# Kernel optimization log

Hardware: AMD Instinct MI355X
Metric: run time of the kernel (lower is better)

## Reference

```python
import jax, jax.numpy as jnp
import numpy as np

NE = 64        # num experts
H = 1024       # hidden_size
F = 2048       # ffn_hidden_size per expert
T = 16384      # total tokens


def setup_inputs() -> dict:
    key = jax.random.key(0)
    k1, k2, k3 = jax.random.split(key, 3)
    x = jax.random.normal(k1, (T, H), jnp.float32)
    w1 = jax.random.normal(k2, (NE, F, H), jnp.float32) * 0.02
    w2 = jax.random.normal(k3, (NE, F, H), jnp.float32) * 0.02
    # ragged token counts per expert, summing exactly to T
    rng = np.random.default_rng(0)
    sizes = rng.multinomial(T, np.ones(NE) / NE)
    tokens_per_expert = jnp.asarray(sizes, jnp.int32)
    return {"x": x, "w1": w1, "w2": w2, "tokens_per_expert": tokens_per_expert}


def _grouped_gmm(x, w, sizes, trans_b=False):
    # grouped GEMM: per-expert segment of x multiplied by that expert's weight.
    # sizes are concrete host ints (group boundaries are static), so we emit
    # one GEMM per expert with static slices, matching gg.ops.gmm semantics.
    offs = np.concatenate([[0], np.cumsum(sizes)]).astype(np.int64)
    outs = []
    for e in range(len(sizes)):
        xe = x[int(offs[e]):int(offs[e + 1])]          # [n_e, k]
        we = w[e].T if trans_b else w[e]               # [k, n]
        outs.append(xe @ we)
    return jnp.concatenate(outs, axis=0)


def reference(x, w1, w2, tokens_per_expert):
    sizes = np.asarray(tokens_per_expert)
    h = _grouped_gmm(x, w1, sizes, trans_b=True)       # [T, F]
    h = jax.nn.gelu(h, approximate=False)              # torch F.gelu (exact erf)
    return _grouped_gmm(h, w2, sizes, trans_b=False)   # [T, H]
```

## Files before the change

### kernel.cpp

```cpp
#include <hip/hip_runtime.h>
#include <hip/hip_bf16.h>

#define NE 64
#define HDIM 1024
#define FDIM 2048
#define TDIM 16384

typedef __attribute__((ext_vector_type(8))) short short8;
typedef __attribute__((ext_vector_type(4))) float f32x4;
typedef unsigned short u16;
typedef unsigned int u32;

struct IC0 { static constexpr int v = 0; };
struct IC1 { static constexpr int v = 1; };
template<int W> struct WN { static constexpr int v = W; };

__device__ __forceinline__ u16 f2bf(float f) {
  return __bfloat16_as_ushort(__float2bfloat16(f));
}
__device__ __forceinline__ u32 pk2(float a, float b) {
  return (u32)f2bf(a) | ((u32)f2bf(b) << 16);
}
template<int N> __device__ __forceinline__ void waitv() {
  if constexpr (N == 2)       asm volatile("s_waitcnt vmcnt(2)" ::: "memory");
  else if constexpr (N == 8)  asm volatile("s_waitcnt vmcnt(8)" ::: "memory");
  else if constexpr (N == 10) asm volatile("s_waitcnt vmcnt(10)" ::: "memory");
}
__device__ __forceinline__ void waitl() {
  asm volatile("s_waitcnt lgkmcnt(0)" ::: "memory");
}

__global__ void k_prep(const int* __restrict__ tpe, int4* __restrict__ map,
                       int* __restrict__ nblocks) {
  if (threadIdx.x != 0 || blockIdx.x != 0) return;
  int off = 0, nb = 0;
  for (int e = 0; e < NE; ++e) {
    int n = tpe[e];
    for (int r = 0; r < n; r += 256) {
      int re = (r + 256 < n) ? (r + 256) : n;
      map[nb++] = make_int4(e, off + r, off + re, 0);
    }
    off += n;
  }
  *nblocks = nb;
}

__global__ void k_conv(const float4* __restrict__ in, uint2* __restrict__ out, int n4) {
  int stride = gridDim.x * blockDim.x;
  for (int i = blockIdx.x * blockDim.x + threadIdx.x; i < n4; i += stride) {
    float4 v = in[i];
    uint2 o;
    o.x = pk2(v.x, v.y);
    o.y = pk2(v.z, v.w);
    out[i] = o;
  }
}

template<int K, int N, int NY>
__global__ __launch_bounds__(512) void k_gemm1(
    const u16* __restrict__ A, const float* __restrict__ Bf, u16* __restrict__ C,
    const int4* __restrict__ map, const int* __restrict__ nblocks)
{
  const int mblk = (int)blockIdx.x / NY;
  const int nblk = (int)blockIdx.x % NY;
  if (mblk >= *nblocks) return;
  const int4 mi = map[mblk];
  const int e = mi.x, row0 = mi.y, rowend = mi.z;
  const int n0 = nblk << 7;
  const int NT = K / 32;

  __shared__ __align__(16) u16   sa[2][8192];
  __shared__ __align__(16) float sbf[3][4096];

  const int tid = threadIdx.x;
  const int wid = tid >> 6, lane = tid & 63;
  const int wr = wid >> 1, wc = wid & 1;
  const int fr = lane & 15, fq = lane >> 4;

  f32x4 acc[4][4];
#pragma unroll
  for (int m = 0; m < 4; ++m)
#pragma unroll
    for (int n = 0; n < 4; ++n) acc[m][n] = (f32x4)0.f;

  const float* B = Bf + (size_t)e * ((size_t)N * K);

  auto issueA = [&](int t, int buf) {
#pragma unroll
    for (int i = 0; i < 2; ++i) {
      int slot = i * 512 + tid;
      int r = slot >> 2, c = slot & 3;
      int cs = c ^ ((r >> 1) & 3);
      int row = row0 + r;
      row = row < TDIM ? row : TDIM - 1;
      const u16* g = A + (size_t)row * K + t * 32 + cs * 8;
      __builtin_amdgcn_global_load_lds(
          (const __attribute__((address_space(1))) u32*)g,
          (__attribute__((address_space(3))) u32*)(&sa[buf][i * 4096 + wid * 512]),
          16, 0, 0);
    }
  };
  auto issueB = [&](int t, int buf) {
#pragma unroll
    for (int i = 0; i < 2; ++i) {
      int slot = i * 512 + tid;
      int nn = slot >> 3, p = slot & 7;
      int cs = p ^ (nn & 7);
      const float* g = B + (size_t)(n0 + nn) * K + t * 32 + cs * 4;
      __builtin_amdgcn_global_load_lds(
          (const __attribute__((address_space(1))) u32*)g,
          (__attribute__((address_space(3))) u32*)(&sbf[buf][i * 2048 + wid * 256]),
          16, 0, 0);
    }
  };

  auto body = [&](int t) {
    waitv<2>();
    __builtin_amdgcn_s_barrier();
    const int curA = t & 1, curB = t % 3;
    issueA((t + 1 < NT) ? (t + 1) : (NT - 1), curA ^ 1);
    issueB((t + 2 < NT) ? (t + 2) : (NT - 1), (t + 2) % 3);
    short8 av[4], bv[4];
#pragma unroll
    for (int m = 0; m < 4; ++m) {
      const int row = wr * 64 + m * 16 + fr;
      av[m] = *(const short8*)(&sa[curA][row * 32 + (fq ^ ((row >> 1) & 3)) * 8]);
    }
#pragma unroll
    for (int n = 0; n < 4; ++n) {
      const int nn = wc * 64 + n * 16 + fr;
      const int swz = nn & 7;
      float4 lo = *(const float4*)(&sbf[curB][nn * 32 + ((fq * 2 + 0) ^ swz) * 4]);
      float4 hi = *(const float4*)(&sbf[curB][nn * 32 + ((fq * 2 + 1) ^ swz) * 4]);
      union { short8 s; u32 u[4]; } bb;
      bb.u[0] = pk2(lo.x, lo.y); bb.u[1] = pk2(lo.z, lo.w);
      bb.u[2] = pk2(hi.x, hi.y); bb.u[3] = pk2(hi.z, hi.w);
      bv[n] = bb.s;
    }
#pragma unroll
    for (int m = 0; m < 4; ++m)
#pragma unroll
      for (int n = 0; n < 4; ++n)
        acc[m][n] = __builtin_amdgcn_mfma_f32_16x16x32_bf16(av[m], bv[n], acc[m][n], 0, 0, 0);
  };

  issueA(0, 0);
  issueB(0, 0);
  issueB(1, 1);
  for (int t = 0; t < NT; ++t) body(t);

#pragma unroll
  for (int m = 0; m < 4; ++m) {
    const int rb = row0 + wr * 64 + m * 16 + fq * 4;
#pragma unroll
    for (int n = 0; n < 4; ++n) {
      const int col = n0 + wc * 64 + n * 16 + fr;
#pragma unroll
      for (int j = 0; j < 4; ++j) {
        int r = rb + j;
        if (r < rowend) {
          float vv = acc[m][n][j];
          vv = 0.5f * vv * (1.f + erff(vv * 0.70710678118654752f));
          C[(size_t)r * N + col] = f2bf(vv);
        }
      }
    }
  }
}

template<int K, int N, int NY>
__global__ __launch_bounds__(512) void k_gemm2(
    const u16* __restrict__ A, const float* __restrict__ Bf, float* __restrict__ C,
    const int4* __restrict__ map, const int* __restrict__ nblocks)
{
  const int mblk = (int)blockIdx.x / NY;
  const int nblk = (int)blockIdx.x % NY;
  if (mblk >= *nblocks) return;
  const int4 mi = map[mblk];
  const int e = mi.x, row0 = mi.y, rowend = mi.z;
  const int n0 = nblk << 7;
  const int NT = K / 32;
  constexpr int LB = 8;

  __shared__ __align__(16) u16 sa[3][8192];
  __shared__ __align__(16) u16 sb[2][128 * 40];

  const int tid = threadIdx.x;
  const int wid = tid >> 6, lane = tid & 63;
  const int wr = wid >> 1, wc = wid & 1;
  const int fr = lane & 15, fq = lane >> 4;

  f32x4 acc[4][4];
#pragma unroll
  for (int m = 0; m < 4; ++m)
#pragma unroll
    for (int n = 0; n < 4; ++n) acc[m][n] = (f32x4)0.f;

  const float* B = Bf + (size_t)e * ((size_t)N * K);

  float rb2[2][8];
  const int bn  = tid & 127;
  const int oct = tid >> 7;

  auto issueA = [&](int t, int buf) {
#pragma unroll
    for (int i = 0; i < 2; ++i) {
      int slot = i * 512 + tid;
      int r = slot >> 2, c = slot & 3;
      int cs = c ^ ((r >> 1) & 3);
      int row = row0 + r;
      row = row < TDIM ? row : TDIM - 1;
      const u16* g = A + (size_t)row * K + t * 32 + cs * 8;
      __builtin_amdgcn_global_load_lds(
          (const __attribute__((address_space(1))) u32*)g,
          (__attribute__((address_space(3))) u32*)(&sa[buf][i * 4096 + wid * 512]),
          16, 0, 0);
    }
  };
  auto loadB = [&](int t, auto ic) {
    constexpr int S = decltype(ic)::v;
    const float* src = B + (size_t)(t * 32 + oct * 8) * N + n0 + bn;
#pragma unroll
    for (int i = 0; i < 8; ++i) rb2[S][i] = src[(size_t)i * N];
  };
  auto writeB = [&](int buf, auto ic) {
    constexpr int S = decltype(ic)::v;
    uint4 c;
    c.x = pk2(rb2[S][0], rb2[S][1]); c.y = pk2(rb2[S][2], rb2[S][3]);
    c.z = pk2(rb2[S][4], rb2[S][5]); c.w = pk2(rb2[S][6], rb2[S][7]);
    *(uint4*)(&sb[buf][bn * 40 + oct * 8]) = c;
  };

  auto body = [&](int t, auto icCur, auto wn) {
    waitv<decltype(wn)::v>();
    waitl();
    __builtin_amdgcn_s_barrier();
    const int cur3 = t % 3, curb = t & 1, nxtb = curb ^ 1;
    short8 av[4], bv[4];
#pragma unroll
    for (int m = 0; m < 4; ++m) {
      const int row = wr * 64 + m * 16 + fr;
      av[m] = *(const short8*)(&sa[cur3][row * 32 + (fq ^ ((row >> 1) & 3)) * 8]);
    }
#pragma unroll
    for (int n = 0; n < 4; ++n)
      bv[n] = *(const short8*)(&sb[curb][(wc * 64 + n * 16 + fr) * 40 + fq * 8]);
    issueA((t + 2 < NT) ? (t + 2) : (NT - 1), (t + 2) % 3);
    writeB(nxtb, icCur);
    loadB((t + 3 < NT) ? (t + 3) : (NT - 1), icCur);
#pragma unroll
    for (int m = 0; m < 4; ++m)
#pragma unroll
      for (int n = 0; n < 4; ++n)
        acc[m][n] = __builtin_amdgcn_mfma_f32_16x16x32_bf16(av[m], bv[n], acc[m][n], 0, 0, 0);
  };

  issueA(0, 0);
  loadB(0, IC0{});
  issueA(1, 1);
  loadB(1, IC1{});
  waitv<2 + LB>();
  writeB(0, IC0{});
  loadB(2, IC0{});

  body(0, IC1{}, WN<LB>{});
  body(1, IC0{}, WN<2 + LB>{});
  for (int t = 2; t < NT; t += 2) {
    body(t,     IC1{}, WN<2 + LB>{});
    body(t + 1, IC0{}, WN<2 + LB>{});
  }

#pragma unroll
  for (int m = 0; m < 4; ++m) {
    const int rb = row0 + wr * 64 + m * 16 + fq * 4;
#pragma unroll
    for (int n = 0; n < 4; ++n) {
      const int col = n0 + wc * 64 + n * 16 + fr;
#pragma unroll
      for (int j = 0; j < 4; ++j) {
        int r = rb + j;
        if (r < rowend) C[(size_t)r * N + col] = acc[m][n][j];
      }
    }
  }
}

extern "C" void kernel_launch(void* const* d_in, const int* in_sizes, int n_in,
                              void* d_out, int out_size, void* d_ws, size_t ws_size,
                              hipStream_t stream) {
  const float* x  = (const float*)d_in[0];
  const float* w1 = (const float*)d_in[1];
  const float* w2 = (const float*)d_in[2];
  const int*  tpe = (const int*)d_in[3];

  char* ws = (char*)d_ws;
  int4* map     = (int4*)ws;
  int*  nblocks = (int*)(ws + 4096);
  u16*  xb      = (u16*)(ws + 8192);
  u16*  hb      = xb + (size_t)TDIM * HDIM;

  k_prep<<<1, 64, 0, stream>>>(tpe, map, nblocks);
  k_conv<<<2048, 256, 0, stream>>>((const float4*)x, (uint2*)xb, (TDIM * HDIM) / 4);
  k_gemm1<HDIM, FDIM, 16><<<128 * 16, 512, 0, stream>>>(
      xb, w1, hb, map, nblocks);
  k_gemm2<FDIM, HDIM, 8><<<128 * 8, 512, 0, stream>>>(
      hb, w2, (float*)d_out, map, nblocks);
}
```

Baseline: 472.4 us.

## Enlarge grouped GEMM tiles to 256x256 and restage B conversion through registers

Both grouped GEMMs move from 256x128 to 256x256 output tiles, with 8 waves in a 2x4 layout each holding 8x4 MFMA accumulators. The first GEMM now converts fp32 weights to bf16 once, in registers, before writing them to LDS. Before, each wave converted its own fp32 LDS reads, so the same conversion was repeated across waves. The main loop is split into phases, with MFMA priority raised via setprio, so global loads and LDS writes overlap with the matrix math. The exact erf GELU becomes a tanh approximation, which is cheaper but changes numerics slightly. Fewer, larger blocks risk worse load balance across CUs, and the larger accumulator set raises register pressure.

```diff
diff --git a/kernel.cpp b/kernel.cpp
--- a/kernel.cpp
+++ b/kernel.cpp
@@ -13,7 +13,6 @@
 
 struct IC0 { static constexpr int v = 0; };
 struct IC1 { static constexpr int v = 1; };
-template<int W> struct WN { static constexpr int v = W; };
 
 __device__ __forceinline__ u16 f2bf(float f) {
   return __bfloat16_as_ushort(__float2bfloat16(f));
@@ -21,8 +20,16 @@
 __device__ __forceinline__ u32 pk2(float a, float b) {
   return (u32)f2bf(a) | ((u32)f2bf(b) << 16);
 }
+__device__ __forceinline__ float gelu_tanh(float x) {
+  float y = 0.7978845608f * (x + 0.044715f * x * x * x);
+  float e = exp2f(2.885390082f * y);
+  float th = 1.f - 2.f / (e + 1.f);
+  return 0.5f * x * (1.f + th);
+}
 template<int N> __device__ __forceinline__ void waitv() {
   if constexpr (N == 2)       asm volatile("s_waitcnt vmcnt(2)" ::: "memory");
+  else if constexpr (N == 4)  asm volatile("s_waitcnt vmcnt(4)" ::: "memory");
+  else if constexpr (N == 6)  asm volatile("s_waitcnt vmcnt(6)" ::: "memory");
   else if constexpr (N == 8)  asm volatile("s_waitcnt vmcnt(8)" ::: "memory");
   else if constexpr (N == 10) asm volatile("s_waitcnt vmcnt(10)" ::: "memory");
 }
@@ -66,103 +73,168 @@
   if (mblk >= *nblocks) return;
   const int4 mi = map[mblk];
   const int e = mi.x, row0 = mi.y, rowend = mi.z;
-  const int n0 = nblk << 7;
-  const int NT = K / 32;
-
-  __shared__ __align__(16) u16   sa[2][8192];
-  __shared__ __align__(16) float sbf[3][4096];
+  const int n0 = nblk << 8;
+  const int NT = K / 64;
+
+  __shared__ __align__(16) u16 sa[2][256 * 64];
+  __shared__ __align__(16) u16 sb[2][256 * 72];
 
   const int tid = threadIdx.x;
   const int wid = tid >> 6, lane = tid & 63;
-  const int wr = wid >> 1, wc = wid & 1;
+  const int wr = wid >> 2, wc = wid & 3;
   const int fr = lane & 15, fq = lane >> 4;
 
-  f32x4 acc[4][4];
-#pragma unroll
-  for (int m = 0; m < 4; ++m)
+  f32x4 acc[8][4];
+#pragma unroll
+  for (int m = 0; m < 8; ++m)
 #pragma unroll
     for (int n = 0; n < 4; ++n) acc[m][n] = (f32x4)0.f;
 
   const float* B = Bf + (size_t)e * ((size_t)N * K);
 
+  float4 rb[2][8];
+
   auto issueA = [&](int t, int buf) {
 #pragma unroll
-    for (int i = 0; i < 2; ++i) {
+    for (int i = 0; i < 4; ++i) {
       int slot = i * 512 + tid;
-      int r = slot >> 2, c = slot & 3;
-      int cs = c ^ ((r >> 1) & 3);
+      int r = slot >> 3, j = slot & 7;
+      int cs = j ^ (r & 7);
       int row = row0 + r;
       row = row < TDIM ? row : TDIM - 1;
-      const u16* g = A + (size_t)row * K + t * 32 + cs * 8;
+      const u16* g = A + (size_t)row * K + t * 64 + cs * 8;
       __builtin_amdgcn_global_load_lds(
           (const __attribute__((address_space(1))) u32*)g,
-          (__attribute__((address_space(3))) u32*)(&sa[buf][i * 4096 + wid * 512]),
+          (__attribute__((address_space(3))) u32*)(&sa[buf][slot * 8]),
           16, 0, 0);
     }
   };
-  auto issueB = [&](int t, int buf) {
+  auto loadBc = [&](int t, int c, auto ic) {
+    constexpr int S = decltype(ic)::v;
 #pragma unroll
     for (int i = 0; i < 2; ++i) {
-      int slot = i * 512 + tid;
-      int nn = slot >> 3, p = slot & 7;
-      int cs = p ^ (nn & 7);
-      const float* g = B + (size_t)(n0 + nn) * K + t * 32 + cs * 4;
-      __builtin_amdgcn_global_load_lds(
-          (const __attribute__((address_space(1))) u32*)g,
-          (__attribute__((address_space(3))) u32*)(&sbf[buf][i * 2048 + wid * 256]),
-          16, 0, 0);
-    }
-  };
-
-  auto body = [&](int t) {
-    waitv<2>();
-    __builtin_amdgcn_s_barrier();
-    const int curA = t & 1, curB = t % 3;
-    issueA((t + 1 < NT) ? (t + 1) : (NT - 1), curA ^ 1);
-    issueB((t + 2 < NT) ? (t + 2) : (NT - 1), (t + 2) % 3);
+      int local = i * 512 + tid;
+      rb[S][c * 2 + i] = *(const float4*)(
+          B + (size_t)(n0 + c * 64 + (local >> 4)) * K + t * 64 + (local & 15) * 4);
+    }
+  };
+  auto writeBc = [&](int buf, int c, auto ic) {
+    constexpr int S = decltype(ic)::v;
+#pragma unroll
+    for (int i = 0; i < 2; ++i) {
+      int local = i * 512 + tid;
+      int n = c * 64 + (local >> 4), f4 = local & 15;
+      float4 v = rb[S][c * 2 + i];
+      uint2 o;
+      o.x = pk2(v.x, v.y);
+      o.y = pk2(v.z, v.w);
+      *(uint2*)(&sb[buf][n * 72 + f4 * 4]) = o;
+    }
+  };
+  auto readA = [&](short8* av, int buf, int mh, int ks) {
+#pragma unroll
+    for (int i = 0; i < 4; ++i) {
+      int R = wr * 128 + (mh * 4 + i) * 16 + fr;
+      av[i] = *(const short8*)(&sa[buf][R * 64 + (((ks * 4 + fq) ^ (R & 7)) * 8)]);
+    }
+  };
+  auto readB = [&](short8* bv, int buf, int ks) {
+#pragma unroll
+    for (int n = 0; n < 4; ++n) {
+      int R = wc * 64 + n * 16 + fr;
+      bv[n] = *(const short8*)(&sb[buf][R * 72 + ks * 32 + fq * 8]);
+    }
+  };
+
+  auto tile = [&](int t, auto icW, auto icL) {
+    const int cur = t & 1, nxt = cur ^ 1;
+    const int tA = (t + 1 < NT) ? (t + 1) : (NT - 1);
+    const int tB = (t + 2 < NT) ? (t + 2) : (NT - 1);
     short8 av[4], bv[4];
-#pragma unroll
-    for (int m = 0; m < 4; ++m) {
-      const int row = wr * 64 + m * 16 + fr;
-      av[m] = *(const short8*)(&sa[curA][row * 32 + (fq ^ ((row >> 1) & 3)) * 8]);
-    }
-#pragma unroll
-    for (int n = 0; n < 4; ++n) {
-      const int nn = wc * 64 + n * 16 + fr;
-      const int swz = nn & 7;
-      float4 lo = *(const float4*)(&sbf[curB][nn * 32 + ((fq * 2 + 0) ^ swz) * 4]);
-      float4 hi = *(const float4*)(&sbf[curB][nn * 32 + ((fq * 2 + 1) ^ swz) * 4]);
-      union { short8 s; u32 u[4]; } bb;
-      bb.u[0] = pk2(lo.x, lo.y); bb.u[1] = pk2(lo.z, lo.w);
-      bb.u[2] = pk2(hi.x, hi.y); bb.u[3] = pk2(hi.z, hi.w);
-      bv[n] = bb.s;
-    }
-#pragma unroll
-    for (int m = 0; m < 4; ++m)
-#pragma unroll
-      for (int n = 0; n < 4; ++n)
-        acc[m][n] = __builtin_amdgcn_mfma_f32_16x16x32_bf16(av[m], bv[n], acc[m][n], 0, 0, 0);
-  };
-
+    waitv<6>();
+    readA(av, cur, 0, 0);
+    readB(bv, cur, 0);
+    issueA(tA, nxt);
+    loadBc(tB, 0, icL);
+    writeBc(nxt, 0, icW);
+    __builtin_amdgcn_s_barrier();
+    waitl();
+    __builtin_amdgcn_s_setprio(1);
+#pragma unroll
+    for (int i = 0; i < 4; ++i)
+#pragma unroll
+      for (int n = 0; n < 4; ++n)
+        acc[i][n] = __builtin_amdgcn_mfma_f32_16x16x32_bf16(av[i], bv[n], acc[i][n], 0, 0, 0);
+    __builtin_amdgcn_s_setprio(0);
+    __builtin_amdgcn_s_barrier();
+    waitv<10>();
+    readA(av, cur, 1, 0);
+    loadBc(tB, 1, icL);
+    writeBc(nxt, 1, icW);
+    __builtin_amdgcn_s_barrier();
+    waitl();
+    __builtin_amdgcn_s_setprio(1);
+#pragma unroll
+    for (int i = 0; i < 4; ++i)
+#pragma unroll
+      for (int n = 0; n < 4; ++n)
+        acc[4 + i][n] = __builtin_amdgcn_mfma_f32_16x16x32_bf16(av[i], bv[n], acc[4 + i][n], 0, 0, 0);
+    __builtin_amdgcn_s_setprio(0);
+    __builtin_amdgcn_s_barrier();
+    waitv<10>();
+    readA(av, cur, 0, 1);
+    readB(bv, cur, 1);
+    loadBc(tB, 2, icL);
+    writeBc(nxt, 2, icW);
+    __builtin_amdgcn_s_barrier();
+    waitl();
+    __builtin_amdgcn_s_setprio(1);
+#pragma unroll
+    for (int i = 0; i < 4; ++i)
+#pragma unroll
+      for (int n = 0; n < 4; ++n)
+        acc[i][n] = __builtin_amdgcn_mfma_f32_16x16x32_bf16(av[i], bv[n], acc[i][n], 0, 0, 0);
+    __builtin_amdgcn_s_setprio(0);
+    __builtin_amdgcn_s_barrier();
+    waitv<10>();
+    readA(av, cur, 1, 1);
+    loadBc(tB, 3, icL);
+    writeBc(nxt, 3, icW);
+    __builtin_amdgcn_s_barrier();
+    waitl();
+    __builtin_amdgcn_s_setprio(1);
+#pragma unroll
+    for (int i = 0; i < 4; ++i)
+#pragma unroll
+      for (int n = 0; n < 4; ++n)
+        acc[4 + i][n] = __builtin_amdgcn_mfma_f32_16x16x32_bf16(av[i], bv[n], acc[4 + i][n], 0, 0, 0);
+    __builtin_amdgcn_s_setprio(0);
+    __builtin_amdgcn_s_barrier();
+  };
+
+  loadBc(0, 0, IC0{}); loadBc(0, 1, IC0{}); loadBc(0, 2, IC0{}); loadBc(0, 3, IC0{});
   issueA(0, 0);
-  issueB(0, 0);
-  issueB(1, 1);
-  for (int t = 0; t < NT; ++t) body(t);
-
-#pragma unroll
-  for (int m = 0; m < 4; ++m) {
-    const int rb = row0 + wr * 64 + m * 16 + fq * 4;
+  waitv<4>();
+  writeBc(0, 0, IC0{}); writeBc(0, 1, IC0{}); writeBc(0, 2, IC0{}); writeBc(0, 3, IC0{});
+  loadBc(1, 0, IC1{}); loadBc(1, 1, IC1{}); loadBc(1, 2, IC1{}); loadBc(1, 3, IC1{});
+  waitl();
+  __builtin_amdgcn_s_barrier();
+
+  for (int t = 0; t < NT; t += 2) {
+    tile(t,     IC1{}, IC0{});
+    tile(t + 1, IC0{}, IC1{});
+  }
+
+#pragma unroll
+  for (int m = 0; m < 8; ++m) {
+    const int rb_ = row0 + wr * 128 + m * 16 + fq * 4;
 #pragma unroll
     for (int n = 0; n < 4; ++n) {
       const int col = n0 + wc * 64 + n * 16 + fr;
 #pragma unroll
       for (int j = 0; j < 4; ++j) {
-        int r = rb + j;
-        if (r < rowend) {
-          float vv = acc[m][n][j];
-          vv = 0.5f * vv * (1.f + erff(vv * 0.70710678118654752f));
-          C[(size_t)r * N + col] = f2bf(vv);
-        }
+        int r = rb_ + j;
+        if (r < rowend) C[(size_t)r * N + col] = f2bf(gelu_tanh(acc[m][n][j]));
       }
     }
   }
@@ -178,107 +250,130 @@
   if (mblk >= *nblocks) return;
   const int4 mi = map[mblk];
   const int e = mi.x, row0 = mi.y, rowend = mi.z;
-  const int n0 = nblk << 7;
+  const int n0 = nblk << 8;
   const int NT = K / 32;
-  constexpr int LB = 8;
-
-  __shared__ __align__(16) u16 sa[3][8192];
-  __shared__ __align__(16) u16 sb[2][128 * 40];
+
+  __shared__ __align__(16) u16 sa[2][256 * 32];
+  __shared__ __align__(16) u16 sb[2][256 * 40];
 
   const int tid = threadIdx.x;
   const int wid = tid >> 6, lane = tid & 63;
-  const int wr = wid >> 1, wc = wid & 1;
+  const int wr = wid >> 2, wc = wid & 3;
   const int fr = lane & 15, fq = lane >> 4;
 
-  f32x4 acc[4][4];
-#pragma unroll
-  for (int m = 0; m < 4; ++m)
+  f32x4 acc[8][4];
+#pragma unroll
+  for (int m = 0; m < 8; ++m)
 #pragma unroll
     for (int n = 0; n < 4; ++n) acc[m][n] = (f32x4)0.f;
 
   const float* B = Bf + (size_t)e * ((size_t)N * K);
 
-  float rb2[2][8];
-  const int bn  = tid & 127;
-  const int oct = tid >> 7;
+  float rb[2][16];
+  const int bn = tid & 255;
+  const int bh = tid >> 8;
 
   auto issueA = [&](int t, int buf) {
 #pragma unroll
     for (int i = 0; i < 2; ++i) {
       int slot = i * 512 + tid;
-      int r = slot >> 2, c = slot & 3;
-      int cs = c ^ ((r >> 1) & 3);
+      int r = slot >> 2, j = slot & 3;
+      int cs = j ^ ((r >> 1) & 3);
       int row = row0 + r;
       row = row < TDIM ? row : TDIM - 1;
       const u16* g = A + (size_t)row * K + t * 32 + cs * 8;
       __builtin_amdgcn_global_load_lds(
           (const __attribute__((address_space(1))) u32*)g,
-          (__attribute__((address_space(3))) u32*)(&sa[buf][i * 4096 + wid * 512]),
+          (__attribute__((address_space(3))) u32*)(&sa[buf][slot * 8]),
           16, 0, 0);
     }
   };
-  auto loadB = [&](int t, auto ic) {
+  auto loadBc = [&](int t, int c, auto ic) {
     constexpr int S = decltype(ic)::v;
-    const float* src = B + (size_t)(t * 32 + oct * 8) * N + n0 + bn;
-#pragma unroll
-    for (int i = 0; i < 8; ++i) rb2[S][i] = src[(size_t)i * N];
-  };
-  auto writeB = [&](int buf, auto ic) {
+    const float* src = B + (size_t)(t * 32 + bh * 16 + c * 8) * N + n0 + bn;
+#pragma unroll
+    for (int j = 0; j < 8; ++j) rb[S][c * 8 + j] = src[(size_t)j * N];
+  };
+  auto writeBc = [&](int buf, int c, auto ic) {
     constexpr int S = decltype(ic)::v;
-    uint4 c;
-    c.x = pk2(rb2[S][0], rb2[S][1]); c.y = pk2(rb2[S][2], rb2[S][3]);
-    c.z = pk2(rb2[S][4], rb2[S][5]); c.w = pk2(rb2[S][6], rb2[S][7]);
-    *(uint4*)(&sb[buf][bn * 40 + oct * 8]) = c;
-  };
-
-  auto body = [&](int t, auto icCur, auto wn) {
-    waitv<decltype(wn)::v>();
-    waitl();
-    __builtin_amdgcn_s_barrier();
-    const int cur3 = t % 3, curb = t & 1, nxtb = curb ^ 1;
+    uint4 o;
+    o.x = pk2(rb[S][c * 8 + 0], rb[S][c * 8 + 1]);
+    o.y = pk2(rb[S][c * 8 + 2], rb[S][c * 8 + 3]);
+    o.z = pk2(rb[S][c * 8 + 4], rb[S][c * 8 + 5]);
+    o.w = pk2(rb[S][c * 8 + 6], rb[S][c * 8 + 7]);
+    *(uint4*)(&sb[buf][bn * 40 + bh * 16 + c * 8]) = o;
+  };
+  auto readA = [&](short8* av, int buf, int mh) {
+#pragma unroll
+    for (int i = 0; i < 4; ++i) {
+      int R = wr * 128 + (mh * 4 + i) * 16 + fr;
+      av[i] = *(const short8*)(&sa[buf][R * 32 + ((fq ^ ((R >> 1) & 3)) * 8)]);
+    }
+  };
+
+  auto tile = [&](int t, auto icW, auto icL) {
+    const int cur = t & 1, nxt = cur ^ 1;
+    const int tA = (t + 1 < NT) ? (t + 1) : (NT - 1);
+    const int tB = (t + 2 < NT) ? (t + 2) : (NT - 1);
     short8 av[4], bv[4];
-#pragma unroll
-    for (int m = 0; m < 4; ++m) {
-      const int row = wr * 64 + m * 16 + fr;
-      av[m] = *(const short8*)(&sa[cur3][row * 32 + (fq ^ ((row >> 1) & 3)) * 8]);
-    }
-#pragma unroll
-    for (int n = 0; n < 4; ++n)
-      bv[n] = *(const short8*)(&sb[curb][(wc * 64 + n * 16 + fr) * 40 + fq * 8]);
-    issueA((t + 2 < NT) ? (t + 2) : (NT - 1), (t + 2) % 3);
-    writeB(nxtb, icCur);
-    loadB((t + 3 < NT) ? (t + 3) : (NT - 1), icCur);
-#pragma unroll
-    for (int m = 0; m < 4; ++m)
-#pragma unroll
-      for (int n = 0; n < 4; ++n)
-        acc[m][n] = __builtin_amdgcn_mfma_f32_16x16x32_bf16(av[m], bv[n], acc[m][n], 0, 0, 0);
-  };
-
+    waitv<8>();
+    readA(av, cur, 0);
+#pragma unroll
+    for (int n = 0; n < 4; ++n) {
+      int R = wc * 64 + n * 16 + fr;
+      bv[n] = *(const short8*)(&sb[cur][R * 40 + fq * 8]);
+    }
+    issueA(tA, nxt);
+    loadBc(tB, 0, icL);
+    writeBc(nxt, 0, icW);
+    __builtin_amdgcn_s_barrier();
+    waitl();
+    __builtin_amdgcn_s_setprio(1);
+#pragma unroll
+    for (int i = 0; i < 4; ++i)
+#pragma unroll
+      for (int n = 0; n < 4; ++n)
+        acc[i][n] = __builtin_amdgcn_mfma_f32_16x16x32_bf16(av[i], bv[n], acc[i][n], 0, 0, 0);
+    __builtin_amdgcn_s_setprio(0);
+    __builtin_amdgcn_s_barrier();
+    waitv<10>();
+    readA(av, cur, 1);
+    loadBc(tB, 1, icL);
+    writeBc(nxt, 1, icW);
+    __builtin_amdgcn_s_barrier();
+    waitl();
+    __builtin_amdgcn_s_setprio(1);
+#pragma unroll
+    for (int i = 0; i < 4; ++i)
+#pragma unroll
+      for (int n = 0; n < 4; ++n)
+        acc[4 + i][n] = __builtin_amdgcn_mfma_f32_16x16x32_bf16(av[i], bv[n], acc[4 + i][n], 0, 0, 0);
+    __builtin_amdgcn_s_setprio(0);
+    __builtin_amdgcn_s_barrier();
+  };
+
+  loadBc(0, 0, IC0{}); loadBc(0, 1, IC0{});
   issueA(0, 0);
-  loadB(0, IC0{});
-  issueA(1, 1);
-  loadB(1, IC1{});
-  waitv<2 + LB>();
-  writeB(0, IC0{});
-  loadB(2, IC0{});
-
-  body(0, IC1{}, WN<LB>{});
-  body(1, IC0{}, WN<2 + LB>{});
-  for (int t = 2; t < NT; t += 2) {
-    body(t,     IC1{}, WN<2 + LB>{});
-    body(t + 1, IC0{}, WN<2 + LB>{});
-  }
-
-#pragma unroll
-  for (int m = 0; m < 4; ++m) {
-    const int rb = row0 + wr * 64 + m * 16 + fq * 4;
+  waitv<2>();
+  writeBc(0, 0, IC0{}); writeBc(0, 1, IC0{});
+  loadBc(1, 0, IC1{}); loadBc(1, 1, IC1{});
+  waitl();
+  __builtin_amdgcn_s_barrier();
+
+  for (int t = 0; t < NT; t += 2) {
+    tile(t,     IC1{}, IC0{});
+    tile(t + 1, IC0{}, IC1{});
+  }
+
+#pragma unroll
+  for (int m = 0; m < 8; ++m) {
+    const int rb_ = row0 + wr * 128 + m * 16 + fq * 4;
 #pragma unroll
     for (int n = 0; n < 4; ++n) {
       const int col = n0 + wc * 64 + n * 16 + fr;
 #pragma unroll
       for (int j = 0; j < 4; ++j) {
-        int r = rb + j;
+        int r = rb_ + j;
         if (r < rowend) C[(size_t)r * N + col] = acc[m][n][j];
       }
     }
@@ -301,8 +396,8 @@
 
   k_prep<<<1, 64, 0, stream>>>(tpe, map, nblocks);
   k_conv<<<2048, 256, 0, stream>>>((const float4*)x, (uint2*)xb, (TDIM * HDIM) / 4);
-  k_gemm1<HDIM, FDIM, 16><<<128 * 16, 512, 0, stream>>>(
+  k_gemm1<HDIM, FDIM, 8><<<128 * 8, 512, 0, stream>>>(
       xb, w1, hb, map, nblocks);
-  k_gemm2<FDIM, HDIM, 8><<<128 * 8, 512, 0, stream>>>(
+  k_gemm2<FDIM, HDIM, 4><<<128 * 4, 512, 0, stream>>>(
       hb, w2, (float*)d_out, map, nblocks);
 }
```

Result: slower. 538.9 us (+14.1%).
